# Performance work log

Measured on AMD Instinct MI355X. Metric: run time of the kernel, lower is better.

## Reference

```python
import jax, jax.numpy as jnp
import numpy as np

N_NODES = 100000
D_IN = 128
D_OUT = 128
N_EDGES = 1600000
BN_EPS = 1e-5


def _glorot(key, fan_in, fan_out):
    limit = np.sqrt(6.0 / (fan_in + fan_out))
    return jax.random.uniform(key, (fan_in, fan_out), jnp.float32, -limit, limit)


def setup_inputs() -> dict:
    key = jax.random.key(0)
    k_x, k_e, k0, k1, k2 = jax.random.split(key, 5)
    x = jax.random.normal(k_x, (N_NODES, D_IN), jnp.float32)
    edge_index = jax.random.randint(k_e, (2, N_EDGES), 0, N_NODES, jnp.int64)
    return {
        "x": x,
        "edge_index": edge_index,
        "kernel": _glorot(k0, D_IN, D_OUT),
        "kernel1": _glorot(k1, D_IN, D_IN),
        "kernel2": _glorot(k2, D_IN, D_IN),
        "gamma": jnp.ones((D_IN,), jnp.float32),
        "beta": jnp.zeros((D_IN,), jnp.float32),
    }


def reference(x, edge_index, kernel, kernel1, kernel2, gamma, beta):
    N = x.shape[0]
    # BatchNorm1d (training mode: batch statistics, biased variance)
    mean = jnp.mean(x, axis=0)
    var = jnp.var(x, axis=0)
    xn = (x - mean) * jax.lax.rsqrt(var + BN_EPS) * gamma + beta

    mapped = xn @ kernel                                  # [N, D_OUT]
    s1 = jnp.tanh(jnp.sum((xn @ kernel1) * xn, axis=1))   # [N]
    s2 = jnp.tanh(jnp.sum((xn @ kernel2) * xn, axis=1))   # [N]

    src, dst = edge_index[0], edge_index[1]
    # edge score: adj values are 1 -> leaky_relu(s1[i] + s2[j]) for edge (i,j)
    e = jax.nn.leaky_relu(s1[src] + s2[dst], negative_slope=0.01)  # [E]

    # sparse row-wise softmax over dim 1 (segment softmax over src)
    emax = jax.ops.segment_max(e, src, num_segments=N)
    emax = jnp.where(jnp.isfinite(emax), emax, 0.0)
    ee = jnp.exp(e - emax[src])
    denom = jax.ops.segment_sum(ee, src, num_segments=N)
    attn = ee / jnp.maximum(denom[src], 1e-16)            # [E]

    # attention_adj @ mapped_inputs (scatter-add over src rows)
    out = jax.ops.segment_sum(attn[:, None] * mapped[dst], src, num_segments=N)
    return jax.nn.relu(out)
```

## Files before the change

kernel.cpp:

```cpp
#include <hip/hip_runtime.h>
#include <math.h>

#define N_NODES 100000
#define D 128
#define N_EDGES 1600000
#define BN_EPS 1e-5f
#define SCAN_NB 200
#define SCAN_BC 500
#define EG_BLOCKS 1563

typedef __attribute__((ext_vector_type(8))) short bf16x8;
typedef __attribute__((ext_vector_type(4))) float f32x4;

__device__ inline unsigned short f2bf(float f) {
    unsigned int u = __float_as_uint(f);
    unsigned int r = u + 0x7FFFu + ((u >> 16) & 1u);
    return (unsigned short)(r >> 16);
}
__device__ inline float bf2f(unsigned short b) {
    return __uint_as_float(((unsigned int)b) << 16);
}

__global__ __launch_bounds__(256)
void bn_stats(const float* __restrict__ x, float* __restrict__ sums) {
    const int col  = threadIdx.x & 127;
    const int half = threadIdx.x >> 7;
    float s = 0.f, sq = 0.f;
    for (int r = blockIdx.x * 2 + half; r < N_NODES; r += gridDim.x * 2) {
        float v = x[(size_t)r * D + col];
        s += v; sq += v * v;
    }
    __shared__ float ls[2][128];
    __shared__ float lq[2][128];
    ls[half][col] = s; lq[half][col] = sq;
    __syncthreads();
    if (threadIdx.x < 128) {
        atomicAdd(&sums[col],       ls[0][col] + ls[1][col]);
        atomicAdd(&sums[128 + col], lq[0][col] + lq[1][col]);
    }
}

__global__ void bn_finalize(const float* __restrict__ sums,
                            const float* __restrict__ gamma,
                            const float* __restrict__ beta,
                            float* __restrict__ scale, float* __restrict__ bias) {
    int c = threadIdx.x;
    float mean = sums[c] * (1.0f / N_NODES);
    float var  = sums[128 + c] * (1.0f / N_NODES) - mean * mean;
    float rstd = rsqrtf(var + BN_EPS);
    float sc = gamma[c] * rstd;
    scale[c] = sc;
    bias[c]  = beta[c] - mean * sc;
}

__global__ __launch_bounds__(256)
void pack_weights(const float* __restrict__ k0, const float* __restrict__ k1,
                  const float* __restrict__ k2, unsigned short* __restrict__ wpack) {
    int idx = blockIdx.x * 256 + threadIdx.x;
    if (idx >= 3 * 4 * 8 * 64) return;
    int m    = idx >> 11;
    int r    = idx & 2047;
    int kk   = r >> 9;
    int r2   = r & 511;
    int nt   = r2 >> 6;
    int lane = r2 & 63;
    const float* W = (m == 0) ? k0 : (m == 1) ? k1 : k2;
    int col   = nt * 16 + (lane & 15);
    int kbase = kk * 32 + (lane >> 4) * 8;
    unsigned int wh[4], wl[4];
#pragma unroll
    for (int i = 0; i < 4; ++i) {
        float a = W[(kbase + 2 * i)     * 128 + col];
        float b = W[(kbase + 2 * i + 1) * 128 + col];
        unsigned short ah = f2bf(a), bh = f2bf(b);
        unsigned short al = f2bf(a - bf2f(ah)), bl = f2bf(b - bf2f(bh));
        wh[i] = (unsigned int)ah | ((unsigned int)bh << 16);
        wl[i] = (unsigned int)al | ((unsigned int)bl << 16);
    }
    uint4* outp = (uint4*)wpack;
    outp[idx]        = make_uint4(wh[0], wh[1], wh[2], wh[3]);
    outp[6144 + idx] = make_uint4(wl[0], wl[1], wl[2], wl[3]);
}

__global__ __launch_bounds__(256, 4)
void gemm_mfma(const float* __restrict__ x, const unsigned short* __restrict__ wpack,
               const float* __restrict__ scale, const float* __restrict__ bias,
               unsigned short* __restrict__ mapped, float* __restrict__ s1,
               float* __restrict__ s2) {
    const int tid  = threadIdx.x;
    const int wave = tid >> 6, lane = tid & 63;
    const int base = blockIdx.x * 64;
    __shared__ unsigned short xbuf[64 * 128];
    char* xb = (char*)xbuf;

    float2 sc = ((const float2*)scale)[lane];
    float2 bs = ((const float2*)bias)[lane];

    unsigned int hipack[16];
#pragma unroll
    for (int rr = 0; rr < 16; ++rr) {
        int row  = wave * 16 + rr;
        int node = base + row;
        float2 v = make_float2(0.f, 0.f);
        if (node < N_NODES) v = ((const float2*)x)[(size_t)node * 64 + lane];
        float f0 = v.x * sc.x + bs.x;
        float f1 = v.y * sc.y + bs.y;
        unsigned short h0 = f2bf(f0), h1 = f2bf(f1);
        unsigned short l0 = f2bf(f0 - bf2f(h0)), l1 = f2bf(f1 - bf2f(h1));
        hipack[rr] = (unsigned int)h0 | ((unsigned int)h1 << 16);
        int byte = (row * 256 + lane * 4) ^ ((row & 7) << 4);
        *(unsigned int*)(xb + byte) = (unsigned int)l0 | ((unsigned int)l1 << 16);
    }
    __syncthreads();

    const int arow  = wave * 16 + (lane & 15);
    const int lrow0 = wave * 16 + (lane >> 4) * 4;

    bf16x8 al[4];
#pragma unroll
    for (int kk = 0; kk < 4; ++kk) {
        int byte = (arow * 256 + kk * 64 + (lane >> 4) * 16) ^ ((arow & 7) << 4);
        al[kk] = *(const bf16x8*)(xb + byte);
    }
    unsigned int xlo[16];
#pragma unroll
    for (int nt = 0; nt < 8; ++nt) {
#pragma unroll
        for (int reg = 0; reg < 4; ++reg) {
            int lrow = lrow0 + reg;
            int col  = nt * 16 + (lane & 15);
            int byte = (lrow * 256 + col * 2) ^ ((lrow & 7) << 4);
            unsigned short v = *(const unsigned short*)(xb + byte);
            int idx = nt * 4 + reg;
            if (idx & 1) xlo[idx >> 1] |= ((unsigned int)v) << 16;
            else         xlo[idx >> 1]  = v;
        }
    }
    __syncthreads();

#pragma unroll
    for (int rr = 0; rr < 16; ++rr) {
        int row  = wave * 16 + rr;
        int byte = (row * 256 + lane * 4) ^ ((row & 7) << 4);
        *(unsigned int*)(xb + byte) = hipack[rr];
    }
    __syncthreads();

    bf16x8 ah[4];
#pragma unroll
    for (int kk = 0; kk < 4; ++kk) {
        int byte = (arow * 256 + kk * 64 + (lane >> 4) * 16) ^ ((arow & 7) << 4);
        ah[kk] = *(const bf16x8*)(xb + byte);
    }

    const bf16x8* wp = (const bf16x8*)wpack;

    {
        f32x4 acc[8] = {};
#pragma unroll
        for (int kk = 0; kk < 4; ++kk) {
#pragma unroll
            for (int nt = 0; nt < 8; ++nt) {
                bf16x8 b = wp[(kk * 8 + nt) * 64 + lane];
                acc[nt] = __builtin_amdgcn_mfma_f32_16x16x32_bf16(ah[kk], b, acc[nt], 0, 0, 0);
            }
        }
        int crow = base + wave * 16 + (lane >> 4) * 4;
        int ccol = lane & 15;
#pragma unroll
        for (int nt = 0; nt < 8; ++nt) {
#pragma unroll
            for (int reg = 0; reg < 4; ++reg) {
                int node = crow + reg;
                if (node < N_NODES)
                    mapped[(size_t)node * 128 + nt * 16 + ccol] = f2bf(acc[nt][reg]);
            }
        }
    }

    {
        float p1[4] = {0.f, 0.f, 0.f, 0.f};
        float p2[4] = {0.f, 0.f, 0.f, 0.f};
#pragma unroll
        for (int nt = 0; nt < 8; ++nt) {
            f32x4 a1 = {0.f, 0.f, 0.f, 0.f};
            f32x4 a2 = {0.f, 0.f, 0.f, 0.f};
#pragma unroll
            for (int kk = 0; kk < 4; ++kk) {
                int fi = (kk * 8 + nt) * 64 + lane;
                bf16x8 b1h = wp[2048 * 1 + fi];
                bf16x8 b1l = wp[6144 + 2048 * 1 + fi];
                bf16x8 b2h = wp[2048 * 2 + fi];
                bf16x8 b2l = wp[6144 + 2048 * 2 + fi];
                a1 = __builtin_amdgcn_mfma_f32_16x16x32_bf16(ah[kk], b1h, a1, 0, 0, 0);
                a1 = __builtin_amdgcn_mfma_f32_16x16x32_bf16(al[kk], b1h, a1, 0, 0, 0);
                a1 = __builtin_amdgcn_mfma_f32_16x16x32_bf16(ah[kk], b1l, a1, 0, 0, 0);
                a2 = __builtin_amdgcn_mfma_f32_16x16x32_bf16(ah[kk], b2h, a2, 0, 0, 0);
                a2 = __builtin_amdgcn_mfma_f32_16x16x32_bf16(al[kk], b2h, a2, 0, 0, 0);
                a2 = __builtin_amdgcn_mfma_f32_16x16x32_bf16(ah[kk], b2l, a2, 0, 0, 0);
            }
            int col = nt * 16 + (lane & 15);
#pragma unroll
            for (int reg = 0; reg < 4; ++reg) {
                int lrow = lrow0 + reg;
                int byte = (lrow * 256 + col * 2) ^ ((lrow & 7) << 4);
                float xh = bf2f(*(const unsigned short*)(xb + byte));
                int idx = nt * 4 + reg;
                unsigned short lo16 = (idx & 1) ? (unsigned short)(xlo[idx >> 1] >> 16)
                                                : (unsigned short)(xlo[idx >> 1] & 0xFFFFu);
                float xv = xh + bf2f(lo16);
                p1[reg] = fmaf(a1[reg], xv, p1[reg]);
                p2[reg] = fmaf(a2[reg], xv, p2[reg]);
            }
        }
#pragma unroll
        for (int reg = 0; reg < 4; ++reg) {
#pragma unroll
            for (int off = 1; off < 16; off <<= 1) {
                p1[reg] += __shfl_xor(p1[reg], off);
                p2[reg] += __shfl_xor(p2[reg], off);
            }
        }
        if ((lane & 15) == 0) {
            int nbase = base + wave * 16 + (lane >> 4) * 4;
#pragma unroll
            for (int reg = 0; reg < 4; ++reg) {
                int node = nbase + reg;
                if (node < N_NODES) {
                    s1[node] = tanhf(p1[reg]);
                    s2[node] = tanhf(p2[reg]);
                }
            }
        }
    }
}

__global__ __launch_bounds__(256)
void hist_rank(const int* __restrict__ src, int* __restrict__ cnt,
               int* __restrict__ rank) {
    const int b = blockIdx.x;
    int* c = cnt + (size_t)(b & 7) * N_NODES;
    const int base = b * 1024 + threadIdx.x;
#pragma unroll
    for (int k = 0; k < 4; ++k) {
        int i = base + k * 256;
        if (i < N_EDGES) rank[i] = atomicAdd(&c[src[i]], 1);
    }
}

__global__ __launch_bounds__(256)
void scan_blocksum(const int* __restrict__ cnt, int* __restrict__ bsum) {
    __shared__ int red[256];
    const int b = blockIdx.x, t = threadIdx.x;
    const int base = b * SCAN_BC;
    int s = 0;
    for (int i = t; i < SCAN_BC; i += 256) {
        int node = base + i;
#pragma unroll
        for (int x = 0; x < 8; ++x) s += cnt[(size_t)x * N_NODES + node];
    }
    red[t] = s;
    __syncthreads();
    for (int off = 128; off; off >>= 1) {
        if (t < off) red[t] += red[t + off];
        __syncthreads();
    }
    if (t == 0) bsum[b] = red[0];
}

__global__ __launch_bounds__(256)
void scan_bases(int* __restrict__ bsum, int* __restrict__ row_off) {
    __shared__ int v[256];
    const int t = threadIdx.x;
    v[t] = (t < SCAN_NB) ? bsum[t] : 0;
    __syncthreads();
    for (int off = 1; off < 256; off <<= 1) {
        int u = (t >= off) ? v[t - off] : 0;
        __syncthreads();
        v[t] += u;
        __syncthreads();
    }
    if (t < SCAN_NB) bsum[t] = (t == 0) ? 0 : v[t - 1];
    if (t == 0) row_off[N_NODES] = v[SCAN_NB - 1];
}

__global__ __launch_bounds__(256)
void scan_write(int* __restrict__ cnt, const int* __restrict__ bsum,
                int* __restrict__ row_off) {
    __shared__ int tsum[256];
    const int b = blockIdx.x, t = threadIdx.x;
    const int i0 = b * SCAN_BC + t * 2;
    int c0[8], c1[8];
    int tot0 = 0, tot1 = 0;
    if (t < 250) {
#pragma unroll
        for (int x = 0; x < 8; ++x) {
            c0[x] = cnt[(size_t)x * N_NODES + i0];
            c1[x] = cnt[(size_t)x * N_NODES + i0 + 1];
            tot0 += c0[x]; tot1 += c1[x];
        }
    }
    tsum[t] = tot0 + tot1;
    __syncthreads();
    for (int off = 1; off < 256; off <<= 1) {
        int u = (t >= off) ? tsum[t - off] : 0;
        __syncthreads();
        tsum[t] += u;
        __syncthreads();
    }
    if (t < 250) {
        int run = bsum[b] + ((t == 0) ? 0 : tsum[t - 1]);
        row_off[i0] = run;
        int acc = run;
#pragma unroll
        for (int x = 0; x < 8; ++x) { cnt[(size_t)x * N_NODES + i0] = acc; acc += c0[x]; }
        run += tot0;
        row_off[i0 + 1] = run;
        acc = run;
#pragma unroll
        for (int x = 0; x < 8; ++x) { cnt[(size_t)x * N_NODES + i0 + 1] = acc; acc += c1[x]; }
    }
}

__global__ __launch_bounds__(256)
void scatter_edges(const int* __restrict__ src, const int* __restrict__ dst,
                   const int* __restrict__ cnt, const int* __restrict__ rank,
                   int* __restrict__ dst_sorted) {
    const int b = blockIdx.x;
    const int* c = cnt + (size_t)(b & 7) * N_NODES;
    const int base = b * 1024 + threadIdx.x;
#pragma unroll
    for (int k = 0; k < 4; ++k) {
        int i = base + k * 256;
        if (i < N_EDGES) dst_sorted[c[src[i]] + rank[i]] = dst[i];
    }
}

__global__ __launch_bounds__(256)
void node_aggregate(const int* __restrict__ row_off, const int* __restrict__ dst_sorted,
                    const float* __restrict__ s1, const float* __restrict__ s2,
                    const unsigned int* __restrict__ mapped,
                    float* __restrict__ out) {
    const int wave = threadIdx.x >> 6, lane = threadIdx.x & 63;
    const int n = blockIdx.x * 4 + wave;
    if (n >= N_NODES) return;
    const int beg = row_off[n], end = row_off[n + 1];
    const int deg = end - beg;
    float acc0 = 0.f, acc1 = 0.f, den = 0.f;

#define GATHER8(WSRC, DSRC, J)                                                   \
    {                                                                            \
        float w0 = __shfl(WSRC, (J) + 0), w1 = __shfl(WSRC, (J) + 1);            \
        float w2 = __shfl(WSRC, (J) + 2), w3 = __shfl(WSRC, (J) + 3);            \
        float w4 = __shfl(WSRC, (J) + 4), w5 = __shfl(WSRC, (J) + 5);            \
        float w6 = __shfl(WSRC, (J) + 6), w7 = __shfl(WSRC, (J) + 7);            \
        int d0 = __shfl(DSRC, (J) + 0), d1 = __shfl(DSRC, (J) + 1);              \
        int d2 = __shfl(DSRC, (J) + 2), d3 = __shfl(DSRC, (J) + 3);              \
        int d4 = __shfl(DSRC, (J) + 4), d5 = __shfl(DSRC, (J) + 5);              \
        int d6 = __shfl(DSRC, (J) + 6), d7 = __shfl(DSRC, (J) + 7);              \
        unsigned int m0 = mapped[(size_t)d0 * 64 + lane];                        \
        unsigned int m1 = mapped[(size_t)d1 * 64 + lane];                        \
        unsigned int m2 = mapped[(size_t)d2 * 64 + lane];                        \
        unsigned int m3 = mapped[(size_t)d3 * 64 + lane];                        \
        unsigned int m4 = mapped[(size_t)d4 * 64 + lane];                        \
        unsigned int m5 = mapped[(size_t)d5 * 64 + lane];                        \
        unsigned int m6 = mapped[(size_t)d6 * 64 + lane];                        \
        unsigned int m7 = mapped[(size_t)d7 * 64 + lane];                        \
        acc0 = fmaf(w0, bf2f((unsigned short)(m0 & 0xFFFFu)), acc0);             \
        acc1 = fmaf(w0, bf2f((unsigned short)(m0 >> 16)), acc1);                 \
        acc0 = fmaf(w1, bf2f((unsigned short)(m1 & 0xFFFFu)), acc0);             \
        acc1 = fmaf(w1, bf2f((unsigned short)(m1 >> 16)), acc1);                 \
        acc0 = fmaf(w2, bf2f((unsigned short)(m2 & 0xFFFFu)), acc0);             \
        acc1 = fmaf(w2, bf2f((unsigned short)(m2 >> 16)), acc1);                 \
        acc0 = fmaf(w3, bf2f((unsigned short)(m3 & 0xFFFFu)), acc0);             \
        acc1 = fmaf(w3, bf2f((unsigned short)(m3 >> 16)), acc1);                 \
        acc0 = fmaf(w4, bf2f((unsigned short)(m4 & 0xFFFFu)), acc0);             \
        acc1 = fmaf(w4, bf2f((unsigned short)(m4 >> 16)), acc1);                 \
        acc0 = fmaf(w5, bf2f((unsigned short)(m5 & 0xFFFFu)), acc0);             \
        acc1 = fmaf(w5, bf2f((unsigned short)(m5 >> 16)), acc1);                 \
        acc0 = fmaf(w6, bf2f((unsigned short)(m6 & 0xFFFFu)), acc0);             \
        acc1 = fmaf(w6, bf2f((unsigned short)(m6 >> 16)), acc1);                 \
        acc0 = fmaf(w7, bf2f((unsigned short)(m7 & 0xFFFFu)), acc0);             \
        acc1 = fmaf(w7, bf2f((unsigned short)(m7 >> 16)), acc1);                 \
    }

    if (deg > 0 && deg <= 64) {
        float s1n = s1[n];
        int   d_l = 0; float e_l = -INFINITY;
        if (lane < deg) {
            d_l = dst_sorted[beg + lane];
            float v = s1n + s2[d_l];
            e_l = v > 0.f ? v : 0.01f * v;
        }
        float m = e_l;
#pragma unroll
        for (int off = 1; off < 64; off <<= 1) m = fmaxf(m, __shfl_xor(m, off));
        float w_l = (lane < deg) ? expf(e_l - m) : 0.f;
        den = w_l;
        int j = 0;
        for (; j + 8 <= deg; j += 8) GATHER8(w_l, d_l, j)
        for (; j < deg; ++j) {
            float wj = __shfl(w_l, j);
            int   dj = __shfl(d_l, j);
            unsigned int mv = mapped[(size_t)dj * 64 + lane];
            acc0 = fmaf(wj, bf2f((unsigned short)(mv & 0xFFFFu)), acc0);
            acc1 = fmaf(wj, bf2f((unsigned short)(mv >> 16)), acc1);
        }
    } else if (deg > 64) {
        float s1n = s1[n];
        float m = -INFINITY;
        for (int chunk = beg; chunk < end; chunk += 64) {
            if (chunk + lane < end) {
                int dj = dst_sorted[chunk + lane];
                float v = s1n + s2[dj];
                m = fmaxf(m, v > 0.f ? v : 0.01f * v);
            }
        }
#pragma unroll
        for (int off = 1; off < 64; off <<= 1) m = fmaxf(m, __shfl_xor(m, off));
        for (int chunk = beg; chunk < end; chunk += 64) {
            int nc = min(64, end - chunk);
            int   d_l = 0; float w_l = 0.f;
            if (lane < nc) {
                d_l = dst_sorted[chunk + lane];
                float v = s1n + s2[d_l];
                float e = v > 0.f ? v : 0.01f * v;
                w_l = expf(e - m);
            }
            den += w_l;
            int j = 0;
            for (; j + 8 <= nc; j += 8) GATHER8(w_l, d_l, j)
            for (; j < nc; ++j) {
                float wj = __shfl(w_l, j);
                int   dj = __shfl(d_l, j);
                unsigned int mv = mapped[(size_t)dj * 64 + lane];
                acc0 = fmaf(wj, bf2f((unsigned short)(mv & 0xFFFFu)), acc0);
                acc1 = fmaf(wj, bf2f((unsigned short)(mv >> 16)), acc1);
            }
        }
    }
#undef GATHER8

    if (deg > 0) {
#pragma unroll
        for (int off = 1; off < 64; off <<= 1) den += __shfl_xor(den, off);
        float inv = 1.f / fmaxf(den, 1e-16f);
        acc0 *= inv; acc1 *= inv;
    }
    ((float2*)out)[(size_t)n * 64 + lane] = make_float2(fmaxf(acc0, 0.f), fmaxf(acc1, 0.f));
}

extern "C" void kernel_launch(void* const* d_in, const int* in_sizes, int n_in,
                              void* d_out, int out_size, void* d_ws, size_t ws_size,
                              hipStream_t stream) {
    const float* x     = (const float*)d_in[0];
    const int*   ei    = (const int*)d_in[1];
    const float* k0    = (const float*)d_in[2];
    const float* k1    = (const float*)d_in[3];
    const float* k2    = (const float*)d_in[4];
    const float* gamma = (const float*)d_in[5];
    const float* beta  = (const float*)d_in[6];
    float* out = (float*)d_out;

    const int* src = ei;
    const int* dst = ei + N_EDGES;

    char* ws = (char*)d_ws;
    unsigned short* wpack = (unsigned short*)ws;           ws += 6 * 128 * 128 * 2;
    float* s1       = (float*)ws;                          ws += N_NODES * 4;
    float* s2       = (float*)ws;                          ws += N_NODES * 4;
    float* scale    = (float*)ws;                          ws += 128 * 4;
    float* bias     = (float*)ws;                          ws += 128 * 4;
    float* sums     = (float*)ws;                          ws += 256 * 4;
    int*   bsum     = (int*)ws;                            ws += 256 * 4;
    int*   row_off  = (int*)ws;                            ws += (N_NODES + 1) * 4;
    int*   cnt      = (int*)ws;                            ws += (size_t)8 * N_NODES * 4;
    int*   rank     = (int*)ws;                            ws += (size_t)N_EDGES * 4;
    int*   dst_sorted = (int*)ws;                          ws += (size_t)N_EDGES * 4;
    unsigned short* mapped = (unsigned short*)ws;          ws += (size_t)N_NODES * D * 2;

    hipMemsetAsync(sums, 0, 256 * sizeof(float), stream);
    hipMemsetAsync(cnt, 0, (size_t)8 * N_NODES * sizeof(int), stream);

    bn_stats<<<256, 256, 0, stream>>>(x, sums);
    bn_finalize<<<1, 128, 0, stream>>>(sums, gamma, beta, scale, bias);
    pack_weights<<<24, 256, 0, stream>>>(k0, k1, k2, wpack);
    gemm_mfma<<<(N_NODES + 63) / 64, 256, 0, stream>>>(x, wpack, scale, bias,
                                                       mapped, s1, s2);
    hist_rank<<<EG_BLOCKS, 256, 0, stream>>>(src, cnt, rank);
    scan_blocksum<<<SCAN_NB, 256, 0, stream>>>(cnt, bsum);
    scan_bases<<<1, 256, 0, stream>>>(bsum, row_off);
    scan_write<<<SCAN_NB, 256, 0, stream>>>(cnt, bsum, row_off);
    scatter_edges<<<EG_BLOCKS, 256, 0, stream>>>(src, dst, cnt, rank, dst_sorted);
    node_aggregate<<<(N_NODES + 3) / 4, 256, 0, stream>>>(row_off, dst_sorted,
                                                          s1, s2,
                                                          (const unsigned int*)mapped,
                                                          out);
}
```

Baseline: 332.6 us.

## Merge independent stages into combined launches to overlap BN, histogram, GEMM and scatter

Independent work is packed into shared launches by splitting on block index. BN statistics run alongside the edge histogram/rank, BN finalize alongside weight packing, and the MFMA GEMM alongside the edge scatter, which cuts the launch count from 10 to 7. The goal is to remove launch gaps and let memory-bound and compute-bound blocks share the GPU. In exchange, the scatter blocks inherit the GEMM's shared-memory allocation and launch bounds, which may lower their occupancy.

```diff
diff --git a/kernel.cpp b/kernel.cpp
--- a/kernel.cpp
+++ b/kernel.cpp
@@ -8,6 +8,7 @@
 #define SCAN_NB 200
 #define SCAN_BC 500
 #define EG_BLOCKS 1563
+#define GEMM_BLOCKS 1563
 
 typedef __attribute__((ext_vector_type(8))) short bf16x8;
 typedef __attribute__((ext_vector_type(4))) float f32x4;
@@ -22,41 +23,56 @@
 }
 
 __global__ __launch_bounds__(256)
-void bn_stats(const float* __restrict__ x, float* __restrict__ sums) {
-    const int col  = threadIdx.x & 127;
-    const int half = threadIdx.x >> 7;
-    float s = 0.f, sq = 0.f;
-    for (int r = blockIdx.x * 2 + half; r < N_NODES; r += gridDim.x * 2) {
-        float v = x[(size_t)r * D + col];
-        s += v; sq += v * v;
-    }
-    __shared__ float ls[2][128];
-    __shared__ float lq[2][128];
-    ls[half][col] = s; lq[half][col] = sq;
-    __syncthreads();
-    if (threadIdx.x < 128) {
-        atomicAdd(&sums[col],       ls[0][col] + ls[1][col]);
-        atomicAdd(&sums[128 + col], lq[0][col] + lq[1][col]);
-    }
-}
-
-__global__ void bn_finalize(const float* __restrict__ sums,
-                            const float* __restrict__ gamma,
-                            const float* __restrict__ beta,
-                            float* __restrict__ scale, float* __restrict__ bias) {
-    int c = threadIdx.x;
-    float mean = sums[c] * (1.0f / N_NODES);
-    float var  = sums[128 + c] * (1.0f / N_NODES) - mean * mean;
-    float rstd = rsqrtf(var + BN_EPS);
-    float sc = gamma[c] * rstd;
-    scale[c] = sc;
-    bias[c]  = beta[c] - mean * sc;
+void stats_hist(const float* __restrict__ x, float* __restrict__ sums,
+                const int* __restrict__ src, int* __restrict__ cnt,
+                int* __restrict__ rank) {
+    if (blockIdx.x < 256) {
+        const int col  = threadIdx.x & 127;
+        const int half = threadIdx.x >> 7;
+        float s = 0.f, sq = 0.f;
+        for (int r = blockIdx.x * 2 + half; r < N_NODES; r += 512) {
+            float v = x[(size_t)r * D + col];
+            s += v; sq += v * v;
+        }
+        __shared__ float ls[2][128];
+        __shared__ float lq[2][128];
+        ls[half][col] = s; lq[half][col] = sq;
+        __syncthreads();
+        if (threadIdx.x < 128) {
+            atomicAdd(&sums[col],       ls[0][col] + ls[1][col]);
+            atomicAdd(&sums[128 + col], lq[0][col] + lq[1][col]);
+        }
+    } else {
+        const int b = blockIdx.x - 256;
+        int* c = cnt + (size_t)(b & 7) * N_NODES;
+        const int base = b * 1024 + threadIdx.x;
+#pragma unroll
+        for (int k = 0; k < 4; ++k) {
+            int i = base + k * 256;
+            if (i < N_EDGES) rank[i] = atomicAdd(&c[src[i]], 1);
+        }
+    }
 }
 
 __global__ __launch_bounds__(256)
-void pack_weights(const float* __restrict__ k0, const float* __restrict__ k1,
-                  const float* __restrict__ k2, unsigned short* __restrict__ wpack) {
-    int idx = blockIdx.x * 256 + threadIdx.x;
+void finalize_pack(const float* __restrict__ sums, const float* __restrict__ gamma,
+                   const float* __restrict__ beta, float* __restrict__ scale,
+                   float* __restrict__ bias,
+                   const float* __restrict__ k0, const float* __restrict__ k1,
+                   const float* __restrict__ k2, unsigned short* __restrict__ wpack) {
+    if (blockIdx.x == 0) {
+        if (threadIdx.x < 128) {
+            int c = threadIdx.x;
+            float mean = sums[c] * (1.0f / N_NODES);
+            float var  = sums[128 + c] * (1.0f / N_NODES) - mean * mean;
+            float rstd = rsqrtf(var + BN_EPS);
+            float sc = gamma[c] * rstd;
+            scale[c] = sc;
+            bias[c]  = beta[c] - mean * sc;
+        }
+        return;
+    }
+    int idx = (blockIdx.x - 1) * 256 + threadIdx.x;
     if (idx >= 3 * 4 * 8 * 64) return;
     int m    = idx >> 11;
     int r    = idx & 2047;
@@ -82,15 +98,103 @@
     outp[6144 + idx] = make_uint4(wl[0], wl[1], wl[2], wl[3]);
 }
 
+__global__ __launch_bounds__(256)
+void scan_blocksum(const int* __restrict__ cnt, int* __restrict__ bsum) {
+    __shared__ int red[256];
+    const int b = blockIdx.x, t = threadIdx.x;
+    const int base = b * SCAN_BC;
+    int s = 0;
+    for (int i = t; i < SCAN_BC; i += 256) {
+        int node = base + i;
+#pragma unroll
+        for (int x = 0; x < 8; ++x) s += cnt[(size_t)x * N_NODES + node];
+    }
+    red[t] = s;
+    __syncthreads();
+    for (int off = 128; off; off >>= 1) {
+        if (t < off) red[t] += red[t + off];
+        __syncthreads();
+    }
+    if (t == 0) bsum[b] = red[0];
+}
+
+__global__ __launch_bounds__(256)
+void scan_bases(int* __restrict__ bsum, int* __restrict__ row_off) {
+    __shared__ int v[256];
+    const int t = threadIdx.x;
+    v[t] = (t < SCAN_NB) ? bsum[t] : 0;
+    __syncthreads();
+    for (int off = 1; off < 256; off <<= 1) {
+        int u = (t >= off) ? v[t - off] : 0;
+        __syncthreads();
+        v[t] += u;
+        __syncthreads();
+    }
+    if (t < SCAN_NB) bsum[t] = (t == 0) ? 0 : v[t - 1];
+    if (t == 0) row_off[N_NODES] = v[SCAN_NB - 1];
+}
+
+__global__ __launch_bounds__(256)
+void scan_write(int* __restrict__ cnt, const int* __restrict__ bsum,
+                int* __restrict__ row_off) {
+    __shared__ int tsum[256];
+    const int b = blockIdx.x, t = threadIdx.x;
+    const int i0 = b * SCAN_BC + t * 2;
+    int c0[8], c1[8];
+    int tot0 = 0, tot1 = 0;
+    if (t < 250) {
+#pragma unroll
+        for (int x = 0; x < 8; ++x) {
+            c0[x] = cnt[(size_t)x * N_NODES + i0];
+            c1[x] = cnt[(size_t)x * N_NODES + i0 + 1];
+            tot0 += c0[x]; tot1 += c1[x];
+        }
+    }
+    tsum[t] = tot0 + tot1;
+    __syncthreads();
+    for (int off = 1; off < 256; off <<= 1) {
+        int u = (t >= off) ? tsum[t - off] : 0;
+        __syncthreads();
+        tsum[t] += u;
+        __syncthreads();
+    }
+    if (t < 250) {
+        int run = bsum[b] + ((t == 0) ? 0 : tsum[t - 1]);
+        row_off[i0] = run;
+        int acc = run;
+#pragma unroll
+        for (int x = 0; x < 8; ++x) { cnt[(size_t)x * N_NODES + i0] = acc; acc += c0[x]; }
+        run += tot0;
+        row_off[i0 + 1] = run;
+        acc = run;
+#pragma unroll
+        for (int x = 0; x < 8; ++x) { cnt[(size_t)x * N_NODES + i0 + 1] = acc; acc += c1[x]; }
+    }
+}
+
 __global__ __launch_bounds__(256, 4)
-void gemm_mfma(const float* __restrict__ x, const unsigned short* __restrict__ wpack,
-               const float* __restrict__ scale, const float* __restrict__ bias,
-               unsigned short* __restrict__ mapped, float* __restrict__ s1,
-               float* __restrict__ s2) {
+void gemm_scatter(const float* __restrict__ x, const unsigned short* __restrict__ wpack,
+                  const float* __restrict__ scale, const float* __restrict__ bias,
+                  unsigned short* __restrict__ mapped, float* __restrict__ s1,
+                  float* __restrict__ s2,
+                  const int* __restrict__ src, const int* __restrict__ dst,
+                  const int* __restrict__ cnt, const int* __restrict__ rank,
+                  int* __restrict__ dst_sorted) {
+    __shared__ unsigned short xbuf[64 * 128];
+    if (blockIdx.x >= GEMM_BLOCKS) {
+        const int b = blockIdx.x - GEMM_BLOCKS;
+        const int* c = cnt + (size_t)(b & 7) * N_NODES;
+        const int base = b * 1024 + threadIdx.x;
+#pragma unroll
+        for (int k = 0; k < 4; ++k) {
+            int i = base + k * 256;
+            if (i < N_EDGES) dst_sorted[c[src[i]] + rank[i]] = dst[i];
+        }
+        return;
+    }
     const int tid  = threadIdx.x;
     const int wave = tid >> 6, lane = tid & 63;
     const int base = blockIdx.x * 64;
-    __shared__ unsigned short xbuf[64 * 128];
     char* xb = (char*)xbuf;
 
     float2 sc = ((const float2*)scale)[lane];
@@ -100,7 +204,7 @@
 #pragma unroll
     for (int rr = 0; rr < 16; ++rr) {
         int row  = wave * 16 + rr;
-        int node = base + row;
+        int node = base + rr + wave * 16;
         float2 v = make_float2(0.f, 0.f);
         if (node < N_NODES) v = ((const float2*)x)[(size_t)node * 64 + lane];
         float f0 = v.x * sc.x + bs.x;
@@ -232,107 +336,6 @@
                 }
             }
         }
-    }
-}
-
-__global__ __launch_bounds__(256)
-void hist_rank(const int* __restrict__ src, int* __restrict__ cnt,
-               int* __restrict__ rank) {
-    const int b = blockIdx.x;
-    int* c = cnt + (size_t)(b & 7) * N_NODES;
-    const int base = b * 1024 + threadIdx.x;
-#pragma unroll
-    for (int k = 0; k < 4; ++k) {
-        int i = base + k * 256;
-        if (i < N_EDGES) rank[i] = atomicAdd(&c[src[i]], 1);
-    }
-}
-
-__global__ __launch_bounds__(256)
-void scan_blocksum(const int* __restrict__ cnt, int* __restrict__ bsum) {
-    __shared__ int red[256];
-    const int b = blockIdx.x, t = threadIdx.x;
-    const int base = b * SCAN_BC;
-    int s = 0;
-    for (int i = t; i < SCAN_BC; i += 256) {
-        int node = base + i;
-#pragma unroll
-        for (int x = 0; x < 8; ++x) s += cnt[(size_t)x * N_NODES + node];
-    }
-    red[t] = s;
-    __syncthreads();
-    for (int off = 128; off; off >>= 1) {
-        if (t < off) red[t] += red[t + off];
-        __syncthreads();
-    }
-    if (t == 0) bsum[b] = red[0];
-}
-
-__global__ __launch_bounds__(256)
-void scan_bases(int* __restrict__ bsum, int* __restrict__ row_off) {
-    __shared__ int v[256];
-    const int t = threadIdx.x;
-    v[t] = (t < SCAN_NB) ? bsum[t] : 0;
-    __syncthreads();
-    for (int off = 1; off < 256; off <<= 1) {
-        int u = (t >= off) ? v[t - off] : 0;
-        __syncthreads();
-        v[t] += u;
-        __syncthreads();
-    }
-    if (t < SCAN_NB) bsum[t] = (t == 0) ? 0 : v[t - 1];
-    if (t == 0) row_off[N_NODES] = v[SCAN_NB - 1];
-}
-
-__global__ __launch_bounds__(256)
-void scan_write(int* __restrict__ cnt, const int* __restrict__ bsum,
-                int* __restrict__ row_off) {
-    __shared__ int tsum[256];
-    const int b = blockIdx.x, t = threadIdx.x;
-    const int i0 = b * SCAN_BC + t * 2;
-    int c0[8], c1[8];
-    int tot0 = 0, tot1 = 0;
-    if (t < 250) {
-#pragma unroll
-        for (int x = 0; x < 8; ++x) {
-            c0[x] = cnt[(size_t)x * N_NODES + i0];
-            c1[x] = cnt[(size_t)x * N_NODES + i0 + 1];
-            tot0 += c0[x]; tot1 += c1[x];
-        }
-    }
-    tsum[t] = tot0 + tot1;
-    __syncthreads();
-    for (int off = 1; off < 256; off <<= 1) {
-        int u = (t >= off) ? tsum[t - off] : 0;
-        __syncthreads();
-        tsum[t] += u;
-        __syncthreads();
-    }
-    if (t < 250) {
-        int run = bsum[b] + ((t == 0) ? 0 : tsum[t - 1]);
-        row_off[i0] = run;
-        int acc = run;
-#pragma unroll
-        for (int x = 0; x < 8; ++x) { cnt[(size_t)x * N_NODES + i0] = acc; acc += c0[x]; }
-        run += tot0;
-        row_off[i0 + 1] = run;
-        acc = run;
-#pragma unroll
-        for (int x = 0; x < 8; ++x) { cnt[(size_t)x * N_NODES + i0 + 1] = acc; acc += c1[x]; }
-    }
-}
-
-__global__ __launch_bounds__(256)
-void scatter_edges(const int* __restrict__ src, const int* __restrict__ dst,
-                   const int* __restrict__ cnt, const int* __restrict__ rank,
-                   int* __restrict__ dst_sorted) {
-    const int b = blockIdx.x;
-    const int* c = cnt + (size_t)(b & 7) * N_NODES;
-    const int base = b * 1024 + threadIdx.x;
-#pragma unroll
-    for (int k = 0; k < 4; ++k) {
-        int i = base + k * 256;
-        if (i < N_EDGES) dst_sorted[c[src[i]] + rank[i]] = dst[i];
     }
 }
 
@@ -482,16 +485,14 @@
     hipMemsetAsync(sums, 0, 256 * sizeof(float), stream);
     hipMemsetAsync(cnt, 0, (size_t)8 * N_NODES * sizeof(int), stream);
 
-    bn_stats<<<256, 256, 0, stream>>>(x, sums);
-    bn_finalize<<<1, 128, 0, stream>>>(sums, gamma, beta, scale, bias);
-    pack_weights<<<24, 256, 0, stream>>>(k0, k1, k2, wpack);
-    gemm_mfma<<<(N_NODES + 63) / 64, 256, 0, stream>>>(x, wpack, scale, bias,
-                                                       mapped, s1, s2);
-    hist_rank<<<EG_BLOCKS, 256, 0, stream>>>(src, cnt, rank);
+    stats_hist<<<256 + EG_BLOCKS, 256, 0, stream>>>(x, sums, src, cnt, rank);
+    finalize_pack<<<25, 256, 0, stream>>>(sums, gamma, beta, scale, bias,
+                                          k0, k1, k2, wpack);
     scan_blocksum<<<SCAN_NB, 256, 0, stream>>>(cnt, bsum);
     scan_bases<<<1, 256, 0, stream>>>(bsum, row_off);
     scan_write<<<SCAN_NB, 256, 0, stream>>>(cnt, bsum, row_off);
-    scatter_edges<<<EG_BLOCKS, 256, 0, stream>>>(src, dst, cnt, rank, dst_sorted);
+    gemm_scatter<<<GEMM_BLOCKS + EG_BLOCKS, 256, 0, stream>>>(
+        x, wpack, scale, bias, mapped, s1, s2, src, dst, cnt, rank, dst_sorted);
     node_aggregate<<<(N_NODES + 3) / 4, 256, 0, stream>>>(row_off, dst_sorted,
                                                           s1, s2,
                                                           (const unsigned int*)mapped,
```

Result: faster. 304.3 us (-8.5%).
